# Kernel tuning notes

Hardware: AMD Instinct MI355X
Metric: run time of the kernel (lower is better)

The kernel has to match this reference:

```python
import jax, jax.numpy as jnp
import numpy as np

C_REG = 50.0  # soft-SVM regularization from __init__ default C=50


def kronecker(A, B):
    # torch: einsum('ab,cd->acbd').view(a*c, b*d)
    return jnp.einsum('ab,cd->acbd', A, B).reshape(
        A.shape[0] * B.shape[0], A.shape[1] * B.shape[1])


def setup_inputs() -> dict:
    key = jax.random.key(0)
    k1, k2, k3, k4 = jax.random.split(key, 4)
    N_c, N_S, N_Q, C, W, H = 16, 25, 15, 3, 32, 32
    D_feat = 640
    S_k = jax.random.normal(k1, (N_c, N_S, C, W, H), dtype=jnp.float32)
    Q_k = jax.random.normal(k2, (N_c, N_Q, C, W, H), dtype=jnp.float32)
    # base_net modeled as Flatten -> Linear(C*W*H, D_feat), no bias
    W_base = jax.random.normal(k3, (C * W * H, D_feat), dtype=jnp.float32) * 0.02
    gamma = jax.random.normal(k4, (1,), dtype=jnp.float32)
    return {"S_k": S_k, "Q_k": Q_k, "W_base": W_base, "gamma": gamma}


def reference(S_k, Q_k, W_base, gamma):
    N_c, N_S = S_k.shape[:2]
    N_Q = Q_k.shape[1]
    # base_net: flatten image dims, project to features
    f_x = S_k.reshape(N_c * N_S, -1) @ W_base  # placeholder
    f_x = Q_k.reshape(N_c * N_Q, -1) @ W_base          # [N_c*N_Q, D]
    K = S_k.reshape(N_c * N_S, -1) @ W_base            # [N_c*N_S, D]
    # kernel matrix + ridge
    aul = K @ K.T + C_REG * jnp.eye(N_c * N_S, dtype=K.dtype)  # [N_c*N_S, N_c*N_S]
    # explicit Kronecker expansion to the full (N_c^2*N_S) system
    Q = kronecker(jnp.eye(N_c, dtype=K.dtype), aul)    # [N_c^2*N_S, N_c^2*N_S]
    p = kronecker(jnp.eye(N_c, dtype=K.dtype),
                  jnp.ones((1, N_S), dtype=K.dtype)).reshape(-1, 1)
    alpha = jnp.linalg.solve(Q, jax.lax.stop_gradient(p))  # p is detached in torch
    alpha = alpha.reshape(N_c, -1)                     # [N_c, N_c*N_S]
    w_k = alpha @ K                                    # [N_c, D]
    logits = -gamma * (f_x @ w_k.T)                    # [N_c*N_Q, N_c]
    return logits
```

## Files before the change

### kernel.cpp

```cpp
#include <hip/hip_runtime.h>
#include <math.h>

#define DIN 3072
#define DF 640
#define MROWS 400
#define QROWS 240
#define NMAT 400
#define PN 416
#define NRHS 16
#define CREG 50.0f
#define PVSTEPS 5
#define CSTEPS 25
#define KSPLIT 4
#define GBLK 13
#define SCOLS 32
#define FPAD 72
#define MTILES 28
#define DPAD 424

typedef __attribute__((ext_vector_type(8))) short bf8v;
typedef __attribute__((ext_vector_type(4))) short s4v;
typedef __attribute__((ext_vector_type(4))) float f32x4;

__device__ __forceinline__ short bf16_rn(float x) {
  unsigned u = __float_as_uint(x);
  u += 0x7FFFu + ((u >> 16) & 1u);
  return (short)(u >> 16);
}
__device__ __forceinline__ void split_sh(float x, short& h, short& l) {
  h = bf16_rn(x);
  float hf = __uint_as_float(((unsigned)(unsigned short)h) << 16);
  l = bf16_rn(x - hf);
}
__device__ __forceinline__ float bf2f(short h) {
  return __uint_as_float(((unsigned)(unsigned short)h) << 16);
}

__global__ __launch_bounds__(256) void gemm_feat_sk(const float* __restrict__ S,
                                                    const float* __restrict__ Qm,
                                                    const float* __restrict__ Wb,
                                                    float* __restrict__ Acc) {
  __shared__ short Ash[64][FPAD];
  __shared__ short Asl[64][FPAD];
  __shared__ short Bsh[64][FPAD];
  __shared__ short Bsl[64][FPAD];
  int tid = threadIdx.x;
  int wave = tid >> 6, lane = tid & 63, l16 = lane & 15, quad = lane >> 4;
  int by = blockIdx.y, bx = blockIdx.x, bz = blockIdx.z;
  int colBase = bx * 64;
  int kbeg = bz * (DIN / KSPLIT), kend = kbeg + (DIN / KSPLIT);
  int kc4 = (tid & 15) * 4;
  float4 ar4[4], br4[4];
  auto load_regs = [&](int kk) {
#pragma unroll
    for (int p = 0; p < 4; ++p) {
      int rowoff = 16 * p;
      const float* srp;
      {
        int ar_ = by * 64 + (tid >> 4) + rowoff;
        srp = (ar_ < MROWS) ? (S + (size_t)ar_ * DIN) : (Qm + (size_t)(ar_ - MROWS) * DIN);
      }
      ar4[p] = *reinterpret_cast<const float4*>(srp + kk + kc4);
      int r = (tid >> 4) + rowoff;
      br4[p] = *reinterpret_cast<const float4*>(Wb + (size_t)(kk + r) * DF + colBase + kc4);
    }
  };
  auto split_write = [&]() {
#pragma unroll
    for (int p = 0; p < 4; ++p) {
      int row = (tid >> 4) + 16 * p;
      s4v hv, lv; short h, l;
      split_sh(ar4[p].x, h, l); hv[0] = h; lv[0] = l;
      split_sh(ar4[p].y, h, l); hv[1] = h; lv[1] = l;
      split_sh(ar4[p].z, h, l); hv[2] = h; lv[2] = l;
      split_sh(ar4[p].w, h, l); hv[3] = h; lv[3] = l;
      *reinterpret_cast<s4v*>(&Ash[row][kc4]) = hv;
      *reinterpret_cast<s4v*>(&Asl[row][kc4]) = lv;
      split_sh(br4[p].x, h, l); Bsh[kc4 + 0][row] = h; Bsl[kc4 + 0][row] = l;
      split_sh(br4[p].y, h, l); Bsh[kc4 + 1][row] = h; Bsl[kc4 + 1][row] = l;
      split_sh(br4[p].z, h, l); Bsh[kc4 + 2][row] = h; Bsl[kc4 + 2][row] = l;
      split_sh(br4[p].w, h, l); Bsh[kc4 + 3][row] = h; Bsl[kc4 + 3][row] = l;
    }
  };
  f32x4 acc[4] = {{0,0,0,0},{0,0,0,0},{0,0,0,0},{0,0,0,0}};
  load_regs(kbeg);
  split_write();
  __syncthreads();
  int k0 = kbeg;
  while (true) {
    int kn = k0 + 64;
    bool more = (kn < kend);
    if (more) load_regs(kn);
#pragma unroll
    for (int kk = 0; kk < 64; kk += 32) {
      int ko = kk + quad * 8;
      bf8v ah = *reinterpret_cast<const bf8v*>(&Ash[wave * 16 + l16][ko]);
      bf8v al = *reinterpret_cast<const bf8v*>(&Asl[wave * 16 + l16][ko]);
#pragma unroll
      for (int t = 0; t < 4; ++t) {
        bf8v bh = *reinterpret_cast<const bf8v*>(&Bsh[t * 16 + l16][ko]);
        bf8v bl = *reinterpret_cast<const bf8v*>(&Bsl[t * 16 + l16][ko]);
        acc[t] = __builtin_amdgcn_mfma_f32_16x16x32_bf16(ah, bh, acc[t], 0, 0, 0);
        acc[t] = __builtin_amdgcn_mfma_f32_16x16x32_bf16(ah, bl, acc[t], 0, 0, 0);
        acc[t] = __builtin_amdgcn_mfma_f32_16x16x32_bf16(al, bh, acc[t], 0, 0, 0);
      }
    }
    if (!more) break;
    __syncthreads();
    split_write();
    __syncthreads();
    k0 = kn;
  }
  float* Ap = Acc + (size_t)bz * 640 * DF;
  int row0 = by * 64 + wave * 16;
#pragma unroll
  for (int t = 0; t < 4; ++t)
#pragma unroll
    for (int r = 0; r < 4; ++r) {
      int row = row0 + quad * 4 + r;
      int col = colBase + t * 16 + l16;
      Ap[(size_t)row * DF + col] = acc[t][r];
    }
}

__global__ __launch_bounds__(256) void feat_reduce(const float* __restrict__ Acc,
                                                   short* __restrict__ Kh,
                                                   short* __restrict__ Kl,
                                                   float* __restrict__ FX,
                                                   float* __restrict__ zbuf,
                                                   float* __restrict__ out) {
  int tid = threadIdx.x;
  if (blockIdx.x == 0) {
    for (int e = tid; e < 16; e += 256) zbuf[e] = 0.f;
  } else if (blockIdx.x == 1) {
    for (int e = tid; e < QROWS * NRHS; e += 256) out[e] = 0.f;
  }
  int idx = blockIdx.x * 256 + tid;
  if (idx >= 640 * DF) return;
  float v = Acc[idx] + Acc[idx + 409600] + Acc[idx + 819200] + Acc[idx + 1228800];
  int row = idx / DF, col = idx - row * DF;
  if (row < MROWS) {
    short h, l; split_sh(v, h, l);
    Kh[(size_t)row * DF + col] = h;
    Kl[(size_t)row * DF + col] = l;
  } else {
    FX[(size_t)(row - MROWS) * DF + col] = v;
  }
}

__global__ __launch_bounds__(256) void gemm_aul(const short* __restrict__ Kh,
                                                const short* __restrict__ Kl,
                                                short* __restrict__ Aph,
                                                short* __restrict__ Apl) {
  int tid = threadIdx.x;
  int wave = tid >> 6, lane = tid & 63;
  int l16 = lane & 15, quad = lane >> 4;
  int row0 = blockIdx.y * 64 + wave * 16;
  int colBase = blockIdx.x * 64;
  bool aValid = (row0 < MROWS);
  const bf8v bzero = {0,0,0,0,0,0,0,0};
  f32x4 acc[4] = {{0,0,0,0},{0,0,0,0},{0,0,0,0},{0,0,0,0}};
  for (int k0 = 0; k0 < DF; k0 += 32) {
    int ka = k0 + quad * 8;
    bf8v ah = bzero, al = bzero;
    if (aValid) {
      size_t ao = (size_t)(row0 + l16) * DF + ka;
      ah = *reinterpret_cast<const bf8v*>(Kh + ao);
      al = *reinterpret_cast<const bf8v*>(Kl + ao);
    }
#pragma unroll
    for (int t = 0; t < 4; ++t) {
      int colt = colBase + t * 16;
      bf8v bh = bzero, bl = bzero;
      if (colt < MROWS) {
        size_t bo = (size_t)(colt + l16) * DF + ka;
        bh = *reinterpret_cast<const bf8v*>(Kh + bo);
        bl = *reinterpret_cast<const bf8v*>(Kl + bo);
      }
      acc[t] = __builtin_amdgcn_mfma_f32_16x16x32_bf16(ah, bh, acc[t], 0, 0, 0);
      acc[t] = __builtin_amdgcn_mfma_f32_16x16x32_bf16(ah, bl, acc[t], 0, 0, 0);
      acc[t] = __builtin_amdgcn_mfma_f32_16x16x32_bf16(al, bh, acc[t], 0, 0, 0);
    }
  }
  if (row0 >= PN) return;
#pragma unroll
  for (int t = 0; t < 4; ++t) {
    int colt = colBase + t * 16;
    if (colt >= PN) continue;
#pragma unroll
    for (int r = 0; r < 4; ++r) {
      int row = row0 + quad * 4 + r;
      int col = colt + l16;
      float v = acc[t][r];
      if (row == col && row < MROWS) v += CREG;
      short h, l; split_sh(v, h, l);
      size_t o = (size_t)row * PN + col;
      Aph[o] = h; Apl[o] = l;
    }
  }
}

__global__ __launch_bounds__(256) void solve_and_m(const short* __restrict__ Aph,
                                                   const short* __restrict__ Apl,
                                                   const float* __restrict__ FX,
                                                   const short* __restrict__ Kh,
                                                   const short* __restrict__ Kl,
                                                   const float* __restrict__ gamma,
                                                   unsigned* __restrict__ D0,
                                                   unsigned* __restrict__ D1,
                                                   float* __restrict__ V0,
                                                   float* __restrict__ V1,
                                                   unsigned* __restrict__ bar,
                                                   unsigned* __restrict__ mflag,
                                                   float* __restrict__ M,
                                                   float* __restrict__ out) {
  int tid = threadIdx.x, b = blockIdx.x;
  int wave = tid >> 6, lane = tid & 63, l16 = lane & 15, quad = lane >> 4;
  const bf8v bzero = {0,0,0,0,0,0,0,0};

  if (b >= GBLK) {
    int mt = b - GBLK;
    int mb = mt / 7, nb = mt - (mt / 7) * 7;
    int q0 = mb * 64 + wave * 16;
    f32x4 acc[4] = {{0,0,0,0},{0,0,0,0},{0,0,0,0},{0,0,0,0}};
    int arow = q0 + l16;
    bool aOk = (arow < QROWS);
    const float* fr = FX + (size_t)(aOk ? arow : 0) * DF;
    for (int k0 = 0; k0 < DF; k0 += 32) {
      int ka = k0 + quad * 8;
      bf8v ah = bzero, al = bzero;
      if (aOk) {
        float4 a0 = *reinterpret_cast<const float4*>(fr + ka);
        float4 a1 = *reinterpret_cast<const float4*>(fr + ka + 4);
        float av[8] = {a0.x, a0.y, a0.z, a0.w, a1.x, a1.y, a1.z, a1.w};
#pragma unroll
        for (int j = 0; j < 8; ++j) { short h, l; split_sh(av[j], h, l); ah[j] = h; al[j] = l; }
      }
#pragma unroll
      for (int t = 0; t < 4; ++t) {
        int n = nb * 64 + t * 16 + l16;
        bf8v bh = bzero, bl = bzero;
        if (n < NMAT) {
          bh = *reinterpret_cast<const bf8v*>(Kh + (size_t)n * DF + ka);
          bl = *reinterpret_cast<const bf8v*>(Kl + (size_t)n * DF + ka);
        }
        acc[t] = __builtin_amdgcn_mfma_f32_16x16x32_bf16(ah, bh, acc[t], 0, 0, 0);
        acc[t] = __builtin_amdgcn_mfma_f32_16x16x32_bf16(ah, bl, acc[t], 0, 0, 0);
        acc[t] = __builtin_amdgcn_mfma_f32_16x16x32_bf16(al, bh, acc[t], 0, 0, 0);
      }
    }
#pragma unroll
    for (int t = 0; t < 4; ++t)
#pragma unroll
      for (int r = 0; r < 4; ++r) {
        int row = q0 + quad * 4 + r;
        int col = nb * 64 + t * 16 + l16;
        if (row < QROWS && col < NMAT)
          __hip_atomic_store(&M[(size_t)row * NMAT + col], acc[t][r],
                             __ATOMIC_RELAXED, __HIP_MEMORY_SCOPE_AGENT);
      }
    __syncthreads();
    if (tid == 0)
      __hip_atomic_fetch_add(mflag, 1u, __ATOMIC_RELEASE, __HIP_MEMORY_SCOPE_AGENT);
    return;
  }

  __shared__ __align__(16) short Abig[2][SCOLS][DPAD];
  __shared__ __align__(16) short dbT[2][NRHS][DPAD];
  __shared__ float yred[4][SCOLS][17];
  __shared__ float vprevL[PN], vcurL[PN];
  __shared__ float XsL[SCOLS][NRHS + 1];
  __shared__ float scal[2];
  __shared__ float rn[4], rd[4];
  int r0 = b * SCOLS;

  for (int e = tid; e < SCOLS * 52; e += 256) {
    int i = e / 52, c = e - i * 52;
    *reinterpret_cast<bf8v*>(&Abig[0][i][c * 8]) =
        *reinterpret_cast<const bf8v*>(Aph + (size_t)(r0 + i) * PN + c * 8);
    *reinterpret_cast<bf8v*>(&Abig[1][i][c * 8]) =
        *reinterpret_cast<const bf8v*>(Apl + (size_t)(r0 + i) * PN + c * 8);
  }
  for (int e = tid; e < NRHS * DPAD; e += 256) (&dbT[0][0][0])[e] = 0;
  for (int e = tid; e < PN; e += 256) {
    float v = (e < NMAT) ? (1.f + 0.125f * (float)(e & 7)) : 0.f;
    vcurL[e] = v;
    dbT[0][0][e] = bf16_rn(v);
  }
  __syncthreads();

  unsigned ph = 0;
  auto gridbar = [&]() {
    __syncthreads();
    ++ph;
    if (tid == 0) {
      unsigned tgt = ph * GBLK;
      __hip_atomic_fetch_add(bar, 1u, __ATOMIC_RELEASE, __HIP_MEMORY_SCOPE_AGENT);
      while (__hip_atomic_load(bar, __ATOMIC_RELAXED, __HIP_MEMORY_SCOPE_AGENT) < tgt)
        __builtin_amdgcn_s_sleep(2);
    }
    __syncthreads();
  };

  auto matvec = [&](bool lo) {
    f32x4 acc0 = {0, 0, 0, 0}, acc1 = {0, 0, 0, 0};
    for (int kt = wave; kt < 13; kt += 4) {
      int ko = kt * 32 + quad * 8;
      bf8v bh = *reinterpret_cast<const bf8v*>(&dbT[0][l16][ko]);
      bf8v ah0 = *reinterpret_cast<const bf8v*>(&Abig[0][l16][ko]);
      bf8v ah1 = *reinterpret_cast<const bf8v*>(&Abig[0][16 + l16][ko]);
      acc0 = __builtin_amdgcn_mfma_f32_16x16x32_bf16(ah0, bh, acc0, 0, 0, 0);
      acc1 = __builtin_amdgcn_mfma_f32_16x16x32_bf16(ah1, bh, acc1, 0, 0, 0);
      if (lo) {
        bf8v bl = *reinterpret_cast<const bf8v*>(&dbT[1][l16][ko]);
        bf8v al0 = *reinterpret_cast<const bf8v*>(&Abig[1][l16][ko]);
        bf8v al1 = *reinterpret_cast<const bf8v*>(&Abig[1][16 + l16][ko]);
        acc0 = __builtin_amdgcn_mfma_f32_16x16x32_bf16(ah0, bl, acc0, 0, 0, 0);
        acc0 = __builtin_amdgcn_mfma_f32_16x16x32_bf16(al0, bh, acc0, 0, 0, 0);
        acc1 = __builtin_amdgcn_mfma_f32_16x16x32_bf16(ah1, bl, acc1, 0, 0, 0);
        acc1 = __builtin_amdgcn_mfma_f32_16x16x32_bf16(al1, bh, acc1, 0, 0, 0);
      }
    }
#pragma unroll
    for (int r_ = 0; r_ < 4; ++r_) {
      yred[wave][quad * 4 + r_][l16] = acc0[r_];
      yred[wave][16 + quad * 4 + r_][l16] = acc1[r_];
    }
  };

  for (int s = 0; s < PVSTEPS; ++s) {
    matvec(false);
    __syncthreads();
    if (tid < SCOLS) {
      float y = yred[0][tid][0] + yred[1][tid][0] + yred[2][tid][0] + yred[3][tid][0];
      float* Vb = (s & 1) ? V1 : V0;
      __hip_atomic_store(&Vb[r0 + tid], y, __ATOMIC_RELAXED, __HIP_MEMORY_SCOPE_AGENT);
    }
    gridbar();
    const float* Vb = (s & 1) ? V1 : V0;
    if (s == PVSTEPS - 1)
      for (int e = tid; e < PN; e += 256) vprevL[e] = vcurL[e];
    float g0 = __hip_atomic_load(&Vb[tid], __ATOMIC_RELAXED, __HIP_MEMORY_SCOPE_AGENT);
    float g1 = (tid < PN - 256)
        ? __hip_atomic_load(&Vb[tid + 256], __ATOMIC_RELAXED, __HIP_MEMORY_SCOPE_AGENT)
        : 0.f;
    {
      float v = g0 * (1.f / 4096.f);
      vcurL[tid] = v;
      dbT[0][0][tid] = bf16_rn(v);
    }
    if (tid < PN - 256) {
      float v = g1 * (1.f / 4096.f);
      vcurL[tid + 256] = v;
      dbT[0][0][tid + 256] = bf16_rn(v);
    }
    __syncthreads();
  }

  {
    float n = 0.f, dd = 0.f;
    for (int e = tid; e < PN; e += 256) {
      n += vprevL[e] * vcurL[e];
      dd += vprevL[e] * vprevL[e];
    }
#pragma unroll
    for (int o = 32; o; o >>= 1) {
      n += __shfl_down(n, o);
      dd += __shfl_down(dd, o);
    }
    if (lane == 0) { rn[wave] = n; rd[wave] = dd; }
    __syncthreads();
    if (tid == 0) {
      float N = rn[0] + rn[1] + rn[2] + rn[3];
      float D = rd[0] + rd[1] + rd[2] + rd[3];
      float rqv = 4096.f * N / D;
      float bb = 1.3f * rqv;
      if (!(bb > 800.f)) bb = 12000.f;
      if (bb > 100000.f) bb = 100000.f;
      scal[0] = 0.5f * (bb + CREG);
      scal[1] = 0.5f * (bb - CREG);
    }
    __syncthreads();
  }
  float theta = scal[0], delta = scal[1];
  float sigma = theta / delta, rho = 1.f / sigma;

  float xr[2], rr[2], dr[2];
#pragma unroll
  for (int m = 0; m < 2; ++m) {
    int rl = (tid >> 4) + 16 * m, c = tid & 15, gi = r0 + rl;
    float pc = (gi < NMAT && (gi / 25) == c) ? 1.f : 0.f;
    xr[m] = 0.f; rr[m] = pc; dr[m] = pc / theta;
    short h, l; split_sh(dr[m], h, l);
    __hip_atomic_store(&D0[(size_t)gi * NRHS + c],
                       ((unsigned)(unsigned short)h << 16) | (unsigned)(unsigned short)l,
                       __ATOMIC_RELAXED, __HIP_MEMORY_SCOPE_AGENT);
  }
  gridbar();
  {
    unsigned gw[26];
#pragma unroll
    for (int j = 0; j < 26; ++j)
      gw[j] = __hip_atomic_load(&D0[tid + 256 * j], __ATOMIC_RELAXED, __HIP_MEMORY_SCOPE_AGENT);
#pragma unroll
    for (int j = 0; j < 26; ++j) {
      int e = tid + 256 * j, row = e >> 4, c = e & 15;
      dbT[0][c][row] = (short)(gw[j] >> 16);
      dbT[1][c][row] = (short)gw[j];
    }
  }
  __syncthreads();

  for (int k = 0; k < CSTEPS - 1; ++k) {
    matvec(true);
    __syncthreads();
    float rho1 = 1.f / (2.f * sigma - rho);
    float s1 = rho1 * rho, s2 = 2.f * rho1 / delta;
    rho = rho1;
    unsigned* Db = (k & 1) ? D0 : D1;
#pragma unroll
    for (int m = 0; m < 2; ++m) {
      int rl = (tid >> 4) + 16 * m, c = tid & 15, gi = r0 + rl;
      float mv = yred[0][rl][c] + yred[1][rl][c] + yred[2][rl][c] + yred[3][rl][c];
      xr[m] += dr[m];
      rr[m] -= mv;
      float dn = s1 * dr[m] + s2 * rr[m];
      dr[m] = dn;
      if (k < CSTEPS - 2) {
        short h, l; split_sh(dn, h, l);
        __hip_atomic_store(&Db[(size_t)gi * NRHS + c],
                           ((unsigned)(unsigned short)h << 16) | (unsigned)(unsigned short)l,
                           __ATOMIC_RELAXED, __HIP_MEMORY_SCOPE_AGENT);
      }
    }
    if (k < CSTEPS - 2) {
      gridbar();
      unsigned gw[26];
#pragma unroll
      for (int j = 0; j < 26; ++j)
        gw[j] = __hip_atomic_load(&Db[tid + 256 * j], __ATOMIC_RELAXED, __HIP_MEMORY_SCOPE_AGENT);
#pragma unroll
      for (int j = 0; j < 26; ++j) {
        int e = tid + 256 * j, row = e >> 4, c = e & 15;
        dbT[0][c][row] = (short)(gw[j] >> 16);
        dbT[1][c][row] = (short)gw[j];
      }
    }
    __syncthreads();
  }

#pragma unroll
  for (int m = 0; m < 2; ++m) {
    int rl = (tid >> 4) + 16 * m, c = tid & 15;
    XsL[rl][c] = xr[m] + dr[m];
  }
  __syncthreads();
  if (tid == 0) {
    while (__hip_atomic_load(mflag, __ATOMIC_RELAXED, __HIP_MEMORY_SCOPE_AGENT) < MTILES)
      __builtin_amdgcn_s_sleep(2);
  }
  __syncthreads();
  float* Msl = reinterpret_cast<float*>(&Abig[0][0][0]);
  {
    float gm[30];
#pragma unroll
    for (int j = 0; j < 30; ++j) {
      int e = tid + 256 * j;
      int q = e >> 5, i = e & 31;
      gm[j] = (r0 + i < NMAT)
                  ? __hip_atomic_load(&M[(size_t)q * NMAT + r0 + i],
                                      __ATOMIC_RELAXED, __HIP_MEMORY_SCOPE_AGENT)
                  : 0.f;
    }
#pragma unroll
    for (int j = 0; j < 30; ++j) Msl[tid + 256 * j] = gm[j];
  }
  __syncthreads();
  float g = -gamma[0];
  int c = tid & 15;
  for (int q = tid >> 4; q < QROWS; q += 16) {
    float s = 0.f;
#pragma unroll
    for (int i = 0; i < SCOLS; ++i) s += Msl[q * SCOLS + i] * XsL[i][c];
    atomicAdd(&out[q * NRHS + c], g * s);
  }
}

extern "C" void kernel_launch(void* const* d_in, const int* in_sizes, int n_in,
                              void* d_out, int out_size, void* d_ws, size_t ws_size,
                              hipStream_t stream) {
  const float* S = (const float*)d_in[0];
  const float* Qm = (const float*)d_in[1];
  const float* Wb = (const float*)d_in[2];
  const float* gamma = (const float*)d_in[3];
  float* out = (float*)d_out;
  char* base = (char*)d_ws;
  short* Kh   = (short*)(base);
  short* Kl   = (short*)(base + 512000);
  float* FX   = (float*)(base + 1024000);
  short* Aph  = (short*)(base + 1638400);
  short* Apl  = (short*)(base + 1984512);
  float* Mm   = (float*)(base + 2330624);
  unsigned* bar = (unsigned*)(base + 2740224);
  unsigned* mflag = (unsigned*)(base + 2740240);
  float* zbuf = (float*)(base + 2740224);
  unsigned* D0 = (unsigned*)(base + 2740288);
  unsigned* D1 = (unsigned*)(base + 2766912);
  float* V0   = (float*)(base + 2793536);
  float* V1   = (float*)(base + 2795200);
  float* Acc  = (float*)(base + 2796864);

  gemm_feat_sk<<<dim3(10, 10, KSPLIT), 256, 0, stream>>>(S, Qm, Wb, Acc);
  feat_reduce<<<1600, 256, 0, stream>>>(Acc, Kh, Kl, FX, zbuf, out);
  gemm_aul<<<dim3(7, 7), 256, 0, stream>>>(Kh, Kl, Aph, Apl);
  solve_and_m<<<GBLK + MTILES, 256, 0, stream>>>(Aph, Apl, FX, Kh, Kl, gamma,
                                                 D0, D1, V0, V1, bar, mflag,
                                                 Mm, out);
}
```

Before: 216.0 us.

## Presplit and transpose W into bf16 hi/lo, drop split-K and reduce pass

A new kernel converts W_base once into transposed bf16 high/low halves. The feature GEMM then reads those halves directly from global memory without LDS staging and runs the full K range per block, so the split-K partial buffer and the separate reduce kernel are gone. The GEMM epilogue now does the bf16 split of K and the FX write itself. The trade-off is fewer blocks (100 instead of 400) with long serial K loops and uncached global B loads with no shared-memory reuse, which may reduce parallelism and latency hiding.

```diff
diff --git a/kernel.cpp b/kernel.cpp
--- a/kernel.cpp
+++ b/kernel.cpp
@@ -11,15 +11,12 @@
 #define CREG 50.0f
 #define PVSTEPS 5
 #define CSTEPS 25
-#define KSPLIT 4
 #define GBLK 13
 #define SCOLS 32
-#define FPAD 72
 #define MTILES 28
 #define DPAD 424
 
 typedef __attribute__((ext_vector_type(8))) short bf8v;
-typedef __attribute__((ext_vector_type(4))) short s4v;
 typedef __attribute__((ext_vector_type(4))) float f32x4;
 
 __device__ __forceinline__ short bf16_rn(float x) {
@@ -32,120 +29,90 @@
   float hf = __uint_as_float(((unsigned)(unsigned short)h) << 16);
   l = bf16_rn(x - hf);
 }
-__device__ __forceinline__ float bf2f(short h) {
-  return __uint_as_float(((unsigned)(unsigned short)h) << 16);
-}
-
-__global__ __launch_bounds__(256) void gemm_feat_sk(const float* __restrict__ S,
-                                                    const float* __restrict__ Qm,
-                                                    const float* __restrict__ Wb,
-                                                    float* __restrict__ Acc) {
-  __shared__ short Ash[64][FPAD];
-  __shared__ short Asl[64][FPAD];
-  __shared__ short Bsh[64][FPAD];
-  __shared__ short Bsl[64][FPAD];
+
+__global__ __launch_bounds__(256) void presplit(const float* __restrict__ Wb,
+                                                short* __restrict__ WTh,
+                                                short* __restrict__ WTl,
+                                                float* __restrict__ zbuf,
+                                                float* __restrict__ out) {
+  int b = blockIdx.x, tid = threadIdx.x;
+  if (b >= 480) {
+    if (b == 480) { if (tid < 16) zbuf[tid] = 0.f; }
+    else { for (int e = tid; e < QROWS * NRHS; e += 256) out[e] = 0.f; }
+    return;
+  }
+  __shared__ short tH[64][68];
+  __shared__ short tL[64][68];
+  int kt = b % 48, ct = b / 48;
+  int k0 = kt * 64, c0 = ct * 64;
+#pragma unroll
+  for (int p = 0; p < 16; ++p) {
+    int idx = p * 256 + tid;
+    int i = idx >> 6, j = idx & 63;
+    float v = Wb[(size_t)(k0 + i) * DF + c0 + j];
+    short h, l; split_sh(v, h, l);
+    tH[i][j] = h; tL[i][j] = l;
+  }
+  __syncthreads();
+#pragma unroll
+  for (int p = 0; p < 16; ++p) {
+    int idx = p * 256 + tid;
+    int j = idx >> 6, i = idx & 63;
+    WTh[(size_t)(c0 + j) * DIN + k0 + i] = tH[i][j];
+    WTl[(size_t)(c0 + j) * DIN + k0 + i] = tL[i][j];
+  }
+}
+
+__global__ __launch_bounds__(256) void gemm_feat(const float* __restrict__ S,
+                                                 const float* __restrict__ Qm,
+                                                 const short* __restrict__ WTh,
+                                                 const short* __restrict__ WTl,
+                                                 short* __restrict__ Kh,
+                                                 short* __restrict__ Kl,
+                                                 float* __restrict__ FX) {
   int tid = threadIdx.x;
   int wave = tid >> 6, lane = tid & 63, l16 = lane & 15, quad = lane >> 4;
-  int by = blockIdx.y, bx = blockIdx.x, bz = blockIdx.z;
-  int colBase = bx * 64;
-  int kbeg = bz * (DIN / KSPLIT), kend = kbeg + (DIN / KSPLIT);
-  int kc4 = (tid & 15) * 4;
-  float4 ar4[4], br4[4];
-  auto load_regs = [&](int kk) {
-#pragma unroll
-    for (int p = 0; p < 4; ++p) {
-      int rowoff = 16 * p;
-      const float* srp;
-      {
-        int ar_ = by * 64 + (tid >> 4) + rowoff;
-        srp = (ar_ < MROWS) ? (S + (size_t)ar_ * DIN) : (Qm + (size_t)(ar_ - MROWS) * DIN);
-      }
-      ar4[p] = *reinterpret_cast<const float4*>(srp + kk + kc4);
-      int r = (tid >> 4) + rowoff;
-      br4[p] = *reinterpret_cast<const float4*>(Wb + (size_t)(kk + r) * DF + colBase + kc4);
-    }
-  };
-  auto split_write = [&]() {
-#pragma unroll
-    for (int p = 0; p < 4; ++p) {
-      int row = (tid >> 4) + 16 * p;
-      s4v hv, lv; short h, l;
-      split_sh(ar4[p].x, h, l); hv[0] = h; lv[0] = l;
-      split_sh(ar4[p].y, h, l); hv[1] = h; lv[1] = l;
-      split_sh(ar4[p].z, h, l); hv[2] = h; lv[2] = l;
-      split_sh(ar4[p].w, h, l); hv[3] = h; lv[3] = l;
-      *reinterpret_cast<s4v*>(&Ash[row][kc4]) = hv;
-      *reinterpret_cast<s4v*>(&Asl[row][kc4]) = lv;
-      split_sh(br4[p].x, h, l); Bsh[kc4 + 0][row] = h; Bsl[kc4 + 0][row] = l;
-      split_sh(br4[p].y, h, l); Bsh[kc4 + 1][row] = h; Bsl[kc4 + 1][row] = l;
-      split_sh(br4[p].z, h, l); Bsh[kc4 + 2][row] = h; Bsl[kc4 + 2][row] = l;
-      split_sh(br4[p].w, h, l); Bsh[kc4 + 3][row] = h; Bsl[kc4 + 3][row] = l;
-    }
-  };
+  int bx = blockIdx.x, by = blockIdx.y;
+  int q0 = by * 64 + wave * 16;
+  int arow = q0 + l16;
+  const float* ar = (arow < MROWS) ? (S + (size_t)arow * DIN)
+                                   : (Qm + (size_t)(arow - MROWS) * DIN);
   f32x4 acc[4] = {{0,0,0,0},{0,0,0,0},{0,0,0,0},{0,0,0,0}};
-  load_regs(kbeg);
-  split_write();
-  __syncthreads();
-  int k0 = kbeg;
-  while (true) {
-    int kn = k0 + 64;
-    bool more = (kn < kend);
-    if (more) load_regs(kn);
-#pragma unroll
-    for (int kk = 0; kk < 64; kk += 32) {
-      int ko = kk + quad * 8;
-      bf8v ah = *reinterpret_cast<const bf8v*>(&Ash[wave * 16 + l16][ko]);
-      bf8v al = *reinterpret_cast<const bf8v*>(&Asl[wave * 16 + l16][ko]);
-#pragma unroll
-      for (int t = 0; t < 4; ++t) {
-        bf8v bh = *reinterpret_cast<const bf8v*>(&Bsh[t * 16 + l16][ko]);
-        bf8v bl = *reinterpret_cast<const bf8v*>(&Bsl[t * 16 + l16][ko]);
-        acc[t] = __builtin_amdgcn_mfma_f32_16x16x32_bf16(ah, bh, acc[t], 0, 0, 0);
-        acc[t] = __builtin_amdgcn_mfma_f32_16x16x32_bf16(ah, bl, acc[t], 0, 0, 0);
-        acc[t] = __builtin_amdgcn_mfma_f32_16x16x32_bf16(al, bh, acc[t], 0, 0, 0);
-      }
-    }
-    if (!more) break;
-    __syncthreads();
-    split_write();
-    __syncthreads();
-    k0 = kn;
-  }
-  float* Ap = Acc + (size_t)bz * 640 * DF;
-  int row0 = by * 64 + wave * 16;
+  for (int k0 = 0; k0 < DIN; k0 += 32) {
+    int ka = k0 + quad * 8;
+    float4 a0 = *reinterpret_cast<const float4*>(ar + ka);
+    float4 a1 = *reinterpret_cast<const float4*>(ar + ka + 4);
+    bf8v ah, al;
+    {
+      float av[8] = {a0.x, a0.y, a0.z, a0.w, a1.x, a1.y, a1.z, a1.w};
+#pragma unroll
+      for (int j = 0; j < 8; ++j) { short h, l; split_sh(av[j], h, l); ah[j] = h; al[j] = l; }
+    }
+#pragma unroll
+    for (int t = 0; t < 4; ++t) {
+      int n = bx * 64 + t * 16 + l16;
+      bf8v bh = *reinterpret_cast<const bf8v*>(WTh + (size_t)n * DIN + ka);
+      bf8v bl = *reinterpret_cast<const bf8v*>(WTl + (size_t)n * DIN + ka);
+      acc[t] = __builtin_amdgcn_mfma_f32_16x16x32_bf16(ah, bh, acc[t], 0, 0, 0);
+      acc[t] = __builtin_amdgcn_mfma_f32_16x16x32_bf16(ah, bl, acc[t], 0, 0, 0);
+      acc[t] = __builtin_amdgcn_mfma_f32_16x16x32_bf16(al, bh, acc[t], 0, 0, 0);
+    }
+  }
 #pragma unroll
   for (int t = 0; t < 4; ++t)
 #pragma unroll
     for (int r = 0; r < 4; ++r) {
-      int row = row0 + quad * 4 + r;
-      int col = colBase + t * 16 + l16;
-      Ap[(size_t)row * DF + col] = acc[t][r];
-    }
-}
-
-__global__ __launch_bounds__(256) void feat_reduce(const float* __restrict__ Acc,
-                                                   short* __restrict__ Kh,
-                                                   short* __restrict__ Kl,
-                                                   float* __restrict__ FX,
-                                                   float* __restrict__ zbuf,
-                                                   float* __restrict__ out) {
-  int tid = threadIdx.x;
-  if (blockIdx.x == 0) {
-    for (int e = tid; e < 16; e += 256) zbuf[e] = 0.f;
-  } else if (blockIdx.x == 1) {
-    for (int e = tid; e < QROWS * NRHS; e += 256) out[e] = 0.f;
-  }
-  int idx = blockIdx.x * 256 + tid;
-  if (idx >= 640 * DF) return;
-  float v = Acc[idx] + Acc[idx + 409600] + Acc[idx + 819200] + Acc[idx + 1228800];
-  int row = idx / DF, col = idx - row * DF;
-  if (row < MROWS) {
-    short h, l; split_sh(v, h, l);
-    Kh[(size_t)row * DF + col] = h;
-    Kl[(size_t)row * DF + col] = l;
-  } else {
-    FX[(size_t)(row - MROWS) * DF + col] = v;
-  }
+      int row = q0 + quad * 4 + r;
+      int col = bx * 64 + t * 16 + l16;
+      float v = acc[t][r];
+      if (row < MROWS) {
+        short h, l; split_sh(v, h, l);
+        Kh[(size_t)row * DF + col] = h;
+        Kl[(size_t)row * DF + col] = l;
+      } else {
+        FX[(size_t)(row - MROWS) * DF + col] = v;
+      }
+    }
 }
 
 __global__ __launch_bounds__(256) void gemm_aul(const short* __restrict__ Kh,
@@ -281,7 +248,9 @@
     *reinterpret_cast<bf8v*>(&Abig[1][i][c * 8]) =
         *reinterpret_cast<const bf8v*>(Apl + (size_t)(r0 + i) * PN + c * 8);
   }
-  for (int e = tid; e < NRHS * DPAD; e += 256) (&dbT[0][0][0])[e] = 0;
+  for (int e = tid; e < NRHS * DPAD; e += 256) {
+    (&dbT[0][0][0])[e] = 0; (&dbT[1][0][0])[e] = 0;
+  }
   for (int e = tid; e < PN; e += 256) {
     float v = (e < NMAT) ? (1.f + 0.125f * (float)(e & 7)) : 0.f;
     vcurL[e] = v;
@@ -340,9 +309,9 @@
     const float* Vb = (s & 1) ? V1 : V0;
     if (s == PVSTEPS - 1)
       for (int e = tid; e < PN; e += 256) vprevL[e] = vcurL[e];
-    float g0 = __hip_atomic_load(&Vb[tid], __ATOMIC_RELAXED, __HIP_MEMORY_SCOPE_AGENT);
+    float g0 = __hip_atomic_load((float*)&Vb[tid], __ATOMIC_RELAXED, __HIP_MEMORY_SCOPE_AGENT);
     float g1 = (tid < PN - 256)
-        ? __hip_atomic_load(&Vb[tid + 256], __ATOMIC_RELAXED, __HIP_MEMORY_SCOPE_AGENT)
+        ? __hip_atomic_load((float*)&Vb[tid + 256], __ATOMIC_RELAXED, __HIP_MEMORY_SCOPE_AGENT)
         : 0.f;
     {
       float v = g0 * (1.f / 4096.f);
@@ -508,10 +477,11 @@
   unsigned* D1 = (unsigned*)(base + 2766912);
   float* V0   = (float*)(base + 2793536);
   float* V1   = (float*)(base + 2795200);
-  float* Acc  = (float*)(base + 2796864);
-
-  gemm_feat_sk<<<dim3(10, 10, KSPLIT), 256, 0, stream>>>(S, Qm, Wb, Acc);
-  feat_reduce<<<1600, 256, 0, stream>>>(Acc, Kh, Kl, FX, zbuf, out);
+  short* WTh  = (short*)(base + 2796864);
+  short* WTl  = (short*)(base + 6729024);
+
+  presplit<<<482, 256, 0, stream>>>(Wb, WTh, WTl, zbuf, out);
+  gemm_feat<<<dim3(10, 10), 256, 0, stream>>>(S, Qm, WTh, WTl, Kh, Kl, FX);
   gemm_aul<<<dim3(7, 7), 256, 0, stream>>>(Kh, Kl, Aph, Apl);
   solve_and_m<<<GBLK + MTILES, 256, 0, stream>>>(Aph, Apl, FX, Kh, Kl, gamma,
                                                  D0, D1, V0, V1, bar, mflag,
```

Measured after the change: 312.6 us. 1.45x slower.
